# Kernel tuning notes

Measured on AMD Instinct MI355X. Metric: run time of the kernel, lower is better.

Reference implementation:

```python
import jax, jax.numpy as jnp
import numpy as np

N_NODES = 100000
N_EDGES = 6400000
N_ELEMENTS = 95  # covalent radii table size
P = 6  # envelope polynomial order (init kwarg p)


def setup_inputs() -> dict:
    key = jax.random.key(0)
    k1, k2, k3, k4 = jax.random.split(key, 4)
    z = jax.random.randint(k1, (N_NODES,), 1, 95)  # atomic numbers 1..94
    edge_distance = jax.random.uniform(k2, (N_EDGES,), jnp.float32, 0.5, 5.0)
    edge_index = jax.random.randint(k3, (2, N_EDGES), 0, N_NODES)
    covalent_radii = jax.random.uniform(k4, (N_ELEMENTS,), jnp.float32, 0.5, 2.0)
    return {
        "z": z,
        "edge_distance": edge_distance,
        "edge_index": edge_index,
        "a_factor": jnp.float32(0.4546),
        "Z_power": jnp.float32(0.0842),
        "screen_coefs": jnp.full((4,), 0.1663, jnp.float32),
        "screen_exps": jnp.full((4,), 0.0354, jnp.float32),
        "covalent_radii": covalent_radii,
    }


def reference(z, edge_distance, edge_index, a_factor, Z_power, screen_coefs, screen_exps, covalent_radii):
    sender, receiver = edge_index[0], edge_index[1]
    Z_u = z[sender]
    Z_v = z[receiver]
    Z_uf = Z_u.astype(edge_distance.dtype)
    Z_vf = Z_v.astype(edge_distance.dtype)

    # screening length a = a_factor * 0.529 / (Zu^zp + Zv^zp)
    a = a_factor * 0.529 / (Z_uf ** Z_power + Z_vf ** Z_power)
    r_over_a = edge_distance / a  # [E]

    # phi(x) = sum_i c_i * exp(-d_i * x)
    phi = jnp.sum(screen_coefs * jnp.exp(-screen_exps * r_over_a[:, None]), axis=-1)  # [E]

    v_edges = 14.3996 * Z_uf * Z_vf / edge_distance * phi

    # smooth cutoff envelope
    r_max = covalent_radii[Z_u] + covalent_radii[Z_v]
    t = edge_distance / r_max
    p = float(P)
    envelope = (1.0
                - (p + 1.0) * (p + 2.0) / 2.0 * t ** P
                + p * (p + 2.0) * t ** (P + 1)
                - p * (p + 1.0) / 2.0 * t ** (P + 2))
    envelope = envelope * (t < 1.0).astype(edge_distance.dtype)

    v_edges = 0.5 * v_edges * envelope

    # scatter-add per receiver node
    V_ZBL = jax.ops.segment_sum(v_edges, receiver, num_segments=z.shape[0])
    return V_ZBL
```

## Files before the change

### kernel.cpp

```cpp
#include <hip/hip_runtime.h>

#define N_ELEM 95
#define MAX_NODES 100096
#define ZW_WORDS (MAX_NODES / 4)
#define RS2 20480
#define MAX_R2 5
#define EBLK 256
#define CAP 4096

typedef float f32x4 __attribute__((ext_vector_type(4)));
typedef int   i32x4 __attribute__((ext_vector_type(4)));
typedef unsigned int u32;
typedef u32 u32x4 __attribute__((ext_vector_type(4)));
typedef unsigned long long u64;
typedef unsigned short u16;

__device__ __forceinline__ u32 bf16_rtn(float f) {
    u32 u = __float_as_uint(f);
    return (u + 0x7FFFu + ((u >> 16) & 1u)) >> 16;
}

__device__ __forceinline__ void build_ztab(
    u32* s_zw, const int* __restrict__ z, int n_words, int n_nodes, int tid, int nthr)
{
    for (int w = tid; w < n_words; w += nthr) {
        const int i = w << 2;
        u32 v;
        if (i + 4 <= n_nodes) {
            const i32x4 zz = ((const i32x4*)z)[w];
            v = ((u32)zz.x & 0xffu) | (((u32)zz.y & 0xffu) << 8)
              | (((u32)zz.z & 0xffu) << 16) | (((u32)zz.w & 0xffu) << 24);
        } else {
            v = 0u;
            for (int k = 0; k < 4 && i + k < n_nodes; ++k)
                v |= ((u32)z[i + k] & 0xffu) << (8 * k);
        }
        s_zw[w] = v;
    }
}

__global__ __launch_bounds__(1024) void k_edge_split(
    const int*   __restrict__ z,
    const float* __restrict__ dist,
    const int*   __restrict__ sender,
    const int*   __restrict__ recv,
    const float* __restrict__ a_factor_p,
    const float* __restrict__ z_power_p,
    const float* __restrict__ coefs,
    const float* __restrict__ exps,
    const float* __restrict__ cradii,
    u32*         __restrict__ seg,
    u32*         __restrict__ counts,
    float*       __restrict__ out,
    int n_edges, int n_words, int n_nodes, int W, int Rr)
{
    __shared__ u32    s_zw[ZW_WORDS];
    __shared__ float2 s_tab[N_ELEM];
    __shared__ float  s_coef[4], s_exp[4], s_inv;
    __shared__ u32    lcur[8];
    __shared__ u32    s_base[16][8];

    const int tid  = threadIdx.x;
    const int lane = tid & 63;
    const int wid  = tid >> 6;

    build_ztab(s_zw, z, n_words, n_nodes, tid, 1024);
    if (tid < N_ELEM) {
        float zp = z_power_p[0];
        s_tab[tid] = make_float2(__powf((float)tid, zp), cradii[tid]);
    }
    if (tid < 4) { s_coef[tid] = coefs[tid]; s_exp[tid] = exps[tid]; }
    if (tid < 8) lcur[tid] = 0u;
    if (tid == 0) s_inv = 1.0f / (a_factor_p[0] * 0.529f);
    __syncthreads();

    const unsigned char* s_zb = (const unsigned char*)s_zw;
    const float inv_pref = s_inv;
    const float c0 = s_coef[0], c1 = s_coef[1], c2 = s_coef[2], c3 = s_coef[3];
    const float e0 = s_exp[0],  e1 = s_exp[1],  e2 = s_exp[2],  e3 = s_exp[3];

    const int n_grp = n_edges >> 3;
    const int b     = blockIdx.x;
    const int g0    = b * W;
    const int g1    = min(n_grp, g0 + W);

    for (int gbase = g0; gbase < g1; gbase += 1024) {
        const int  gg     = gbase + tid;
        const bool active = (gg < g1);
        const int  g      = active ? gg : (g1 - 1);

        const f32x4 dA = ((const f32x4*)dist)[2 * g];
        const f32x4 dB = ((const f32x4*)dist)[2 * g + 1];
        const i32x4 sA = ((const i32x4*)sender)[2 * g];
        const i32x4 sB = ((const i32x4*)sender)[2 * g + 1];
        const i32x4 rA = ((const i32x4*)recv)[2 * g];
        const i32x4 rB = ((const i32x4*)recv)[2 * g + 1];

        float dd[8] = {dA.x, dA.y, dA.z, dA.w, dB.x, dB.y, dB.z, dB.w};
        int   ss[8] = {sA.x, sA.y, sA.z, sA.w, sB.x, sB.y, sB.z, sB.w};
        int   rr[8] = {rA.x, rA.y, rA.z, rA.w, rB.x, rB.y, rB.z, rB.w};

        int zu[8], zv[8];
        #pragma unroll
        for (int k = 0; k < 8; ++k) zu[k] = s_zb[ss[k]];
        #pragma unroll
        for (int k = 0; k < 8; ++k) zv[k] = s_zb[rr[k]];

        bool  em[8];
        float val[8];
        u32   entry[8], rgk[8];
        u64   cnt_pk = 0ull;

        #pragma unroll
        for (int k = 0; k < 8; ++k) {
            const float d = dd[k];
            const float2 tu = s_tab[zu[k]];
            const float2 tv = s_tab[zv[k]];
            const float rmax = tu.y + tv.y;
            em[k] = active && (d < rmax);
            float o = 0.0f;
            if (em[k]) {
                const float t   = __fdividef(d, rmax);
                const float roa = d * (tu.x + tv.x) * inv_pref;
                const float phi = c0 * __expf(-e0 * roa)
                                + c1 * __expf(-e1 * roa)
                                + c2 * __expf(-e2 * roa)
                                + c3 * __expf(-e3 * roa);
                const float v   = 7.1998f * (float)(zu[k] * zv[k]) * phi
                                * __fdividef(1.0f, d);
                const float t2  = t * t;
                const float t6  = t2 * t2 * t2;
                o = v * (1.0f - t6 * (28.0f - 48.0f * t + 21.0f * t2));
            }
            val[k] = o;
            const u32 rv  = (u32)rr[k];
            const u32 rg  = rv / (u32)RS2;
            rgk[k] = rg;
            entry[k] = ((rv - rg * (u32)RS2) << 16) | bf16_rtn(o);
            if (em[k]) cnt_pk += 1ull << (12 * rg);
        }

        u64 v = cnt_pk;
        #pragma unroll
        for (int d = 1; d < 64; d <<= 1) {
            u64 t = __shfl_up(v, (unsigned)d, 64);
            if (lane >= d) v += t;
        }
        const u64 excl = v - cnt_pk;

        if (lane == 63) {
            for (int r = 0; r < Rr; ++r) {
                const u32 tot = (u32)(v >> (12 * r)) & 0xFFFu;
                s_base[wid][r] = tot ? atomicAdd(&lcur[r], tot) : lcur[r];
            }
        }

        u64 run_pk = 0ull;
        #pragma unroll
        for (int k = 0; k < 8; ++k) {
            if (em[k]) {
                const u32 rg  = rgk[k];
                const u32 off = ((u32)(excl >> (12 * rg)) & 0xFFFu)
                              + ((u32)(run_pk >> (12 * rg)) & 0xFFFu);
                run_pk += 1ull << (12 * rg);
                const u32 base = s_base[wid][rg];
                const u32 pos  = base + off;
                if (pos < (u32)CAP)
                    seg[((size_t)b * Rr + rg) * CAP + pos] = entry[k];
                else
                    unsafeAtomicAdd(&out[rr[k]], val[k]);
            }
        }
    }

    if (b == gridDim.x - 1) {
        for (int i = (n_grp << 3) + tid; i < n_edges; i += 1024) {
            const float d  = dist[i];
            const int   a  = s_zb[sender[i]];
            const u32   rv = (u32)recv[i];
            const int   bb = s_zb[rv];
            const float2 tu = s_tab[a];
            const float2 tv = s_tab[bb];
            const float rmax = tu.y + tv.y;
            if (d < rmax) {
                const float t   = __fdividef(d, rmax);
                const float roa = d * (tu.x + tv.x) * inv_pref;
                const float phi = c0 * __expf(-e0 * roa)
                                + c1 * __expf(-e1 * roa)
                                + c2 * __expf(-e2 * roa)
                                + c3 * __expf(-e3 * roa);
                const float v   = 7.1998f * (float)(a * bb) * phi * __fdividef(1.0f, d);
                const float t2  = t * t;
                const float t6  = t2 * t2 * t2;
                const float o   = v * (1.0f - t6 * (28.0f - 48.0f * t + 21.0f * t2));
                const u32 rg    = rv / (u32)RS2;
                const u32 pos   = atomicAdd(&lcur[rg], 1u);
                if (pos < (u32)CAP)
                    seg[((size_t)b * Rr + rg) * CAP + pos] =
                        ((rv - rg * (u32)RS2) << 16) | bf16_rtn(o);
                else
                    unsafeAtomicAdd(&out[rv], o);
            }
        }
    }

    __syncthreads();
    if (tid < Rr)
        counts[b * Rr + tid] = min(lcur[tid], (u32)CAP);
}

__global__ __launch_bounds__(1024, 2) void k_gather_accum(
    const u32* __restrict__ seg,
    const u32* __restrict__ counts,
    u16*       __restrict__ copies,
    int C_acc, int Rr)
{
    __shared__ float acc[RS2];
    const int c = blockIdx.x % C_acc;
    const int r = blockIdx.x / C_acc;
    const int tid = threadIdx.x;

    int b0 = c;
    u32 cnt = (b0 < EBLK) ? counts[b0 * Rr + r] : 0u;

    for (int i = tid; i < RS2; i += 1024) acc[i] = 0.0f;
    __syncthreads();

    for (int b = c; b < EBLK; b += C_acc) {
        const int bn = b + C_acc;
        const u32 cnt_next = (bn < EBLK) ? counts[bn * Rr + r] : 0u;
        const u32* __restrict__ p = seg + ((size_t)b * Rr + r) * CAP;
        for (u32 i = tid; i < cnt; i += 1024) {
            const u32 w = p[i];
            atomicAdd(&acc[w >> 16], __uint_as_float((w & 0xFFFFu) << 16));
        }
        cnt = cnt_next;
    }
    __syncthreads();

    u16* __restrict__ dst = copies + ((size_t)c * Rr + r) * RS2;
    for (int i = tid * 8; i + 8 <= RS2; i += 8192) {
        const f32x4 a = *(const f32x4*)(acc + i);
        const f32x4 b = *(const f32x4*)(acc + i + 4);
        u32x4 o;
        o.x = bf16_rtn(a.x) | (bf16_rtn(a.y) << 16);
        o.y = bf16_rtn(a.z) | (bf16_rtn(a.w) << 16);
        o.z = bf16_rtn(b.x) | (bf16_rtn(b.y) << 16);
        o.w = bf16_rtn(b.z) | (bf16_rtn(b.w) << 16);
        *(u32x4*)(dst + i) = o;
    }
}

__global__ __launch_bounds__(256) void k_final5(
    const u32* __restrict__ copies32, float* __restrict__ out,
    int n_nodes, int C, int RRS32)
{
    const int p = blockIdx.x * 256 + threadIdx.x;
    const int n = p << 1;
    if (n < n_nodes) {
        float s0 = 0.0f, s1 = 0.0f;
        #pragma unroll 8
        for (int c = 0; c < C; ++c) {
            const u32 w = copies32[(size_t)c * RRS32 + p];
            s0 += __uint_as_float(w << 16);
            s1 += __uint_as_float(w & 0xFFFF0000u);
        }
        if (n + 1 < n_nodes) {
            const float2 prev = *(const float2*)(out + n);
            *(float2*)(out + n) = make_float2(prev.x + s0, prev.y + s1);
        } else {
            out[n] += s0;
        }
    }
}

__global__ __launch_bounds__(1024) void zbl_edge_lds(
    const int* __restrict__ z, const float* __restrict__ dist,
    const int* __restrict__ sender, const int* __restrict__ recv,
    const float* __restrict__ a_factor_p, const float* __restrict__ z_power_p,
    const float* __restrict__ coefs, const float* __restrict__ exps,
    const float* __restrict__ cradii, float* __restrict__ out,
    int n_edges, int n_words, int n_nodes)
{
    __shared__ u32    s_zw[ZW_WORDS];
    __shared__ float2 s_tab[N_ELEM];
    __shared__ float  s_coef[4], s_exp[4], s_inv;
    const int tid = threadIdx.x;
    build_ztab(s_zw, z, n_words, n_nodes, tid, 1024);
    if (tid < N_ELEM) {
        float zp = z_power_p[0];
        s_tab[tid] = make_float2(__powf((float)tid, zp), cradii[tid]);
    }
    if (tid < 4) { s_coef[tid] = coefs[tid]; s_exp[tid] = exps[tid]; }
    if (tid == 0) s_inv = 1.0f / (a_factor_p[0] * 0.529f);
    __syncthreads();
    const unsigned char* s_zb = (const unsigned char*)s_zw;
    const float inv_pref = s_inv;
    const int gstride = gridDim.x * 1024;
    for (int i = blockIdx.x * 1024 + tid; i < n_edges; i += gstride) {
        const float d  = dist[i];
        const int   a  = s_zb[sender[i]];
        const int   rv = recv[i];
        const int   b  = s_zb[rv];
        const float2 tu = s_tab[a];
        const float2 tv = s_tab[b];
        const float rmax = tu.y + tv.y;
        if (d < rmax) {
            const float t   = __fdividef(d, rmax);
            const float roa = d * (tu.x + tv.x) * inv_pref;
            const float phi = s_coef[0] * __expf(-s_exp[0] * roa)
                            + s_coef[1] * __expf(-s_exp[1] * roa)
                            + s_coef[2] * __expf(-s_exp[2] * roa)
                            + s_coef[3] * __expf(-s_exp[3] * roa);
            const float v   = 7.1998f * (float)(a * b) * phi * __fdividef(1.0f, d);
            const float t2  = t * t;
            const float t6  = t2 * t2 * t2;
            const float env = 1.0f - t6 * (28.0f - 48.0f * t + 21.0f * t2);
            unsafeAtomicAdd(&out[rv], v * env);
        }
    }
}

static inline size_t align16(size_t x) { return (x + 15) & ~(size_t)15; }

extern "C" void kernel_launch(void* const* d_in, const int* in_sizes, int n_in,
                              void* d_out, int out_size, void* d_ws, size_t ws_size,
                              hipStream_t stream) {
    const int*   z        = (const int*)d_in[0];
    const float* dist     = (const float*)d_in[1];
    const int*   eidx     = (const int*)d_in[2];
    const float* a_factor = (const float*)d_in[3];
    const float* z_power  = (const float*)d_in[4];
    const float* coefs    = (const float*)d_in[5];
    const float* exps     = (const float*)d_in[6];
    const float* cradii   = (const float*)d_in[7];
    float* out = (float*)d_out;

    const int n_edges = in_sizes[1];
    const int n_nodes = out_size;
    const int* sender = eidx;
    const int* recv   = eidx + n_edges;

    const int n_words = (n_nodes + 3) >> 2;
    const int R = (n_nodes + RS2 - 1) / RS2;

    const size_t seg_bytes = (size_t)EBLK * R * CAP * sizeof(u32);
    const size_t off_cnt   = align16(seg_bytes);
    const size_t off_cop   = align16(off_cnt + (size_t)EBLK * R * sizeof(u32));

    int C_acc = 0;
    if (R >= 1 && R <= MAX_R2 && n_nodes <= MAX_NODES) {
        const int opts[4] = {100, 51, 32, 16};
        for (int i = 0; i < 4; ++i) {
            size_t need = off_cop + (size_t)opts[i] * R * RS2 * sizeof(u16);
            if (ws_size >= need) { C_acc = opts[i]; break; }
        }
    }

    hipMemsetAsync(out, 0, (size_t)n_nodes * sizeof(float), stream);

    if (C_acc > 0) {
        char* ws = (char*)d_ws;
        u32* seg    = (u32*)ws;
        u32* counts = (u32*)(ws + off_cnt);
        u16* copies = (u16*)(ws + off_cop);

        const int n_grp = n_edges >> 3;
        const int W = (n_grp + EBLK - 1) / EBLK;

        k_edge_split<<<EBLK, 1024, 0, stream>>>(
            z, dist, sender, recv, a_factor, z_power, coefs, exps, cradii,
            seg, counts, out, n_edges, n_words, n_nodes, W, R);
        k_gather_accum<<<C_acc * R, 1024, 0, stream>>>(seg, counts, copies, C_acc, R);
        k_final5<<<((n_nodes + 1) / 2 + 255) / 256, 256, 0, stream>>>(
            (const u32*)copies, out, n_nodes, C_acc, (R * RS2) >> 1);
    } else if (n_nodes <= MAX_NODES) {
        zbl_edge_lds<<<256, 1024, 0, stream>>>(
            z, dist, sender, recv, a_factor, z_power, coefs, exps, cradii,
            out, n_edges, n_words, n_nodes);
    }
}
```

Measured before the change: 77.43 us.

## Shrink LDS z-table so two 1024-thread blocks fit per CU, double edge blocks

```diff
diff --git a/kernel.cpp b/kernel.cpp
--- a/kernel.cpp
+++ b/kernel.cpp
@@ -2,11 +2,12 @@
 
 #define N_ELEM 95
 #define MAX_NODES 100096
-#define ZW_WORDS (MAX_NODES / 4)
+#define ZSPLIT 80384
+#define ZW_WORDS (ZSPLIT / 4)
 #define RS2 20480
 #define MAX_R2 5
-#define EBLK 256
-#define CAP 4096
+#define EBLK 512
+#define CAP 2048
 
 typedef float f32x4 __attribute__((ext_vector_type(4)));
 typedef int   i32x4 __attribute__((ext_vector_type(4)));
@@ -21,9 +22,9 @@
 }
 
 __device__ __forceinline__ void build_ztab(
-    u32* s_zw, const int* __restrict__ z, int n_words, int n_nodes, int tid, int nthr)
-{
-    for (int w = tid; w < n_words; w += nthr) {
+    u32* s_zw, const int* __restrict__ z, int zw_words, int n_nodes, int tid, int nthr)
+{
+    for (int w = tid; w < zw_words; w += nthr) {
         const int i = w << 2;
         u32 v;
         if (i + 4 <= n_nodes) {
@@ -39,7 +40,7 @@
     }
 }
 
-__global__ __launch_bounds__(1024) void k_edge_split(
+__global__ __launch_bounds__(1024, 2) void k_edge_split(
     const int*   __restrict__ z,
     const float* __restrict__ dist,
     const int*   __restrict__ sender,
@@ -52,25 +53,25 @@
     u32*         __restrict__ seg,
     u32*         __restrict__ counts,
     float*       __restrict__ out,
-    int n_edges, int n_words, int n_nodes, int W, int Rr)
+    int n_edges, int zw_words, int n_nodes, int W, int Rr)
 {
     __shared__ u32    s_zw[ZW_WORDS];
     __shared__ float2 s_tab[N_ELEM];
     __shared__ float  s_coef[4], s_exp[4], s_inv;
-    __shared__ u32    lcur[8];
-    __shared__ u32    s_base[16][8];
+    __shared__ u32    lcur[MAX_R2];
+    __shared__ u32    s_base[16][MAX_R2];
 
     const int tid  = threadIdx.x;
     const int lane = tid & 63;
     const int wid  = tid >> 6;
 
-    build_ztab(s_zw, z, n_words, n_nodes, tid, 1024);
+    build_ztab(s_zw, z, zw_words, n_nodes, tid, 1024);
     if (tid < N_ELEM) {
         float zp = z_power_p[0];
         s_tab[tid] = make_float2(__powf((float)tid, zp), cradii[tid]);
     }
     if (tid < 4) { s_coef[tid] = coefs[tid]; s_exp[tid] = exps[tid]; }
-    if (tid < 8) lcur[tid] = 0u;
+    if (tid < MAX_R2) lcur[tid] = 0u;
     if (tid == 0) s_inv = 1.0f / (a_factor_p[0] * 0.529f);
     __syncthreads();
 
@@ -102,9 +103,15 @@
 
         int zu[8], zv[8];
         #pragma unroll
-        for (int k = 0; k < 8; ++k) zu[k] = s_zb[ss[k]];
-        #pragma unroll
-        for (int k = 0; k < 8; ++k) zv[k] = s_zb[rr[k]];
+        for (int k = 0; k < 8; ++k) {
+            const int i = ss[k];
+            zu[k] = (i < ZSPLIT) ? (int)s_zb[i] : z[i];
+        }
+        #pragma unroll
+        for (int k = 0; k < 8; ++k) {
+            const int i = rr[k];
+            zv[k] = (i < ZSPLIT) ? (int)s_zb[i] : z[i];
+        }
 
         bool  em[8];
         float val[8];
@@ -176,9 +183,10 @@
     if (b == gridDim.x - 1) {
         for (int i = (n_grp << 3) + tid; i < n_edges; i += 1024) {
             const float d  = dist[i];
-            const int   a  = s_zb[sender[i]];
+            const int   si = sender[i];
             const u32   rv = (u32)recv[i];
-            const int   bb = s_zb[rv];
+            const int   a  = (si < ZSPLIT) ? (int)s_zb[si] : z[si];
+            const int   bb = ((int)rv < ZSPLIT) ? (int)s_zb[rv] : z[rv];
             const float2 tu = s_tab[a];
             const float2 tv = s_tab[bb];
             const float rmax = tu.y + tv.y;
@@ -220,8 +228,7 @@
     const int r = blockIdx.x / C_acc;
     const int tid = threadIdx.x;
 
-    int b0 = c;
-    u32 cnt = (b0 < EBLK) ? counts[b0 * Rr + r] : 0u;
+    u32 cnt = (c < EBLK) ? counts[c * Rr + r] : 0u;
 
     for (int i = tid; i < RS2; i += 1024) acc[i] = 0.0f;
     __syncthreads();
@@ -274,19 +281,19 @@
     }
 }
 
-__global__ __launch_bounds__(1024) void zbl_edge_lds(
+__global__ __launch_bounds__(1024, 2) void zbl_edge_lds(
     const int* __restrict__ z, const float* __restrict__ dist,
     const int* __restrict__ sender, const int* __restrict__ recv,
     const float* __restrict__ a_factor_p, const float* __restrict__ z_power_p,
     const float* __restrict__ coefs, const float* __restrict__ exps,
     const float* __restrict__ cradii, float* __restrict__ out,
-    int n_edges, int n_words, int n_nodes)
+    int n_edges, int zw_words, int n_nodes)
 {
     __shared__ u32    s_zw[ZW_WORDS];
     __shared__ float2 s_tab[N_ELEM];
     __shared__ float  s_coef[4], s_exp[4], s_inv;
     const int tid = threadIdx.x;
-    build_ztab(s_zw, z, n_words, n_nodes, tid, 1024);
+    build_ztab(s_zw, z, zw_words, n_nodes, tid, 1024);
     if (tid < N_ELEM) {
         float zp = z_power_p[0];
         s_tab[tid] = make_float2(__powf((float)tid, zp), cradii[tid]);
@@ -299,9 +306,10 @@
     const int gstride = gridDim.x * 1024;
     for (int i = blockIdx.x * 1024 + tid; i < n_edges; i += gstride) {
         const float d  = dist[i];
-        const int   a  = s_zb[sender[i]];
+        const int   si = sender[i];
         const int   rv = recv[i];
-        const int   b  = s_zb[rv];
+        const int   a  = (si < ZSPLIT) ? (int)s_zb[si] : z[si];
+        const int   b  = (rv < ZSPLIT) ? (int)s_zb[rv] : z[rv];
         const float2 tu = s_tab[a];
         const float2 tv = s_tab[b];
         const float rmax = tu.y + tv.y;
@@ -341,7 +349,7 @@
     const int* sender = eidx;
     const int* recv   = eidx + n_edges;
 
-    const int n_words = (n_nodes + 3) >> 2;
+    const int zw_words = (min(n_nodes, ZSPLIT) + 3) >> 2;
     const int R = (n_nodes + RS2 - 1) / RS2;
 
     const size_t seg_bytes = (size_t)EBLK * R * CAP * sizeof(u32);
@@ -370,13 +378,13 @@
 
         k_edge_split<<<EBLK, 1024, 0, stream>>>(
             z, dist, sender, recv, a_factor, z_power, coefs, exps, cradii,
-            seg, counts, out, n_edges, n_words, n_nodes, W, R);
+            seg, counts, out, n_edges, zw_words, n_nodes, W, R);
         k_gather_accum<<<C_acc * R, 1024, 0, stream>>>(seg, counts, copies, C_acc, R);
         k_final5<<<((n_nodes + 1) / 2 + 255) / 256, 256, 0, stream>>>(
             (const u32*)copies, out, n_nodes, C_acc, (R * RS2) >> 1);
     } else if (n_nodes <= MAX_NODES) {
-        zbl_edge_lds<<<256, 1024, 0, stream>>>(
+        zbl_edge_lds<<<512, 1024, 0, stream>>>(
             z, dist, sender, recv, a_factor, z_power, coefs, exps, cradii,
-            out, n_edges, n_words, n_nodes);
-    }
-}
+            out, n_edges, zw_words, n_nodes);
+    }
+}
```

Measured after the change: 94.82 us. +22.5%, slower.

## Software-prefetch next edge group in split kernel and halve accumulator copies

Applied to the files above, without the earlier changes.

```diff
diff --git a/kernel.cpp b/kernel.cpp
--- a/kernel.cpp
+++ b/kernel.cpp
@@ -57,8 +57,8 @@
     __shared__ u32    s_zw[ZW_WORDS];
     __shared__ float2 s_tab[N_ELEM];
     __shared__ float  s_coef[4], s_exp[4], s_inv;
-    __shared__ u32    lcur[8];
-    __shared__ u32    s_base[16][8];
+    __shared__ u32    lcur[MAX_R2];
+    __shared__ u32    s_base[16][MAX_R2];
 
     const int tid  = threadIdx.x;
     const int lane = tid & 63;
@@ -70,7 +70,7 @@
         s_tab[tid] = make_float2(__powf((float)tid, zp), cradii[tid]);
     }
     if (tid < 4) { s_coef[tid] = coefs[tid]; s_exp[tid] = exps[tid]; }
-    if (tid < 8) lcur[tid] = 0u;
+    if (tid < MAX_R2) lcur[tid] = 0u;
     if (tid == 0) s_inv = 1.0f / (a_factor_p[0] * 0.529f);
     __syncthreads();
 
@@ -84,92 +84,107 @@
     const int g0    = b * W;
     const int g1    = min(n_grp, g0 + W);
 
-    for (int gbase = g0; gbase < g1; gbase += 1024) {
-        const int  gg     = gbase + tid;
-        const bool active = (gg < g1);
-        const int  g      = active ? gg : (g1 - 1);
-
-        const f32x4 dA = ((const f32x4*)dist)[2 * g];
-        const f32x4 dB = ((const f32x4*)dist)[2 * g + 1];
-        const i32x4 sA = ((const i32x4*)sender)[2 * g];
-        const i32x4 sB = ((const i32x4*)sender)[2 * g + 1];
-        const i32x4 rA = ((const i32x4*)recv)[2 * g];
-        const i32x4 rB = ((const i32x4*)recv)[2 * g + 1];
-
-        float dd[8] = {dA.x, dA.y, dA.z, dA.w, dB.x, dB.y, dB.z, dB.w};
-        int   ss[8] = {sA.x, sA.y, sA.z, sA.w, sB.x, sB.y, sB.z, sB.w};
-        int   rr[8] = {rA.x, rA.y, rA.z, rA.w, rB.x, rB.y, rB.z, rB.w};
-
-        int zu[8], zv[8];
-        #pragma unroll
-        for (int k = 0; k < 8; ++k) zu[k] = s_zb[ss[k]];
-        #pragma unroll
-        for (int k = 0; k < 8; ++k) zv[k] = s_zb[rr[k]];
-
-        bool  em[8];
-        float val[8];
-        u32   entry[8], rgk[8];
-        u64   cnt_pk = 0ull;
-
-        #pragma unroll
-        for (int k = 0; k < 8; ++k) {
-            const float d = dd[k];
-            const float2 tu = s_tab[zu[k]];
-            const float2 tv = s_tab[zv[k]];
-            const float rmax = tu.y + tv.y;
-            em[k] = active && (d < rmax);
-            float o = 0.0f;
-            if (em[k]) {
-                const float t   = __fdividef(d, rmax);
-                const float roa = d * (tu.x + tv.x) * inv_pref;
-                const float phi = c0 * __expf(-e0 * roa)
-                                + c1 * __expf(-e1 * roa)
-                                + c2 * __expf(-e2 * roa)
-                                + c3 * __expf(-e3 * roa);
-                const float v   = 7.1998f * (float)(zu[k] * zv[k]) * phi
-                                * __fdividef(1.0f, d);
-                const float t2  = t * t;
-                const float t6  = t2 * t2 * t2;
-                o = v * (1.0f - t6 * (28.0f - 48.0f * t + 21.0f * t2));
-            }
-            val[k] = o;
-            const u32 rv  = (u32)rr[k];
-            const u32 rg  = rv / (u32)RS2;
-            rgk[k] = rg;
-            entry[k] = ((rv - rg * (u32)RS2) << 16) | bf16_rtn(o);
-            if (em[k]) cnt_pk += 1ull << (12 * rg);
-        }
-
-        u64 v = cnt_pk;
-        #pragma unroll
-        for (int d = 1; d < 64; d <<= 1) {
-            u64 t = __shfl_up(v, (unsigned)d, 64);
-            if (lane >= d) v += t;
-        }
-        const u64 excl = v - cnt_pk;
-
-        if (lane == 63) {
-            for (int r = 0; r < Rr; ++r) {
-                const u32 tot = (u32)(v >> (12 * r)) & 0xFFFu;
-                s_base[wid][r] = tot ? atomicAdd(&lcur[r], tot) : lcur[r];
-            }
-        }
-
-        u64 run_pk = 0ull;
-        #pragma unroll
-        for (int k = 0; k < 8; ++k) {
-            if (em[k]) {
-                const u32 rg  = rgk[k];
-                const u32 off = ((u32)(excl >> (12 * rg)) & 0xFFFu)
-                              + ((u32)(run_pk >> (12 * rg)) & 0xFFFu);
-                run_pk += 1ull << (12 * rg);
-                const u32 base = s_base[wid][rg];
-                const u32 pos  = base + off;
-                if (pos < (u32)CAP)
-                    seg[((size_t)b * Rr + rg) * CAP + pos] = entry[k];
-                else
-                    unsafeAtomicAdd(&out[rr[k]], val[k]);
-            }
+    if (g0 < g1) {
+        const int n_iter = (g1 - g0 + 1023) >> 10;
+
+        int  gg  = g0 + tid;
+        bool act = (gg < g1);
+        int  g   = act ? gg : (g1 - 1);
+        f32x4 dA = ((const f32x4*)dist)[2 * g];
+        f32x4 dB = ((const f32x4*)dist)[2 * g + 1];
+        i32x4 sA = ((const i32x4*)sender)[2 * g];
+        i32x4 sB = ((const i32x4*)sender)[2 * g + 1];
+        i32x4 rA = ((const i32x4*)recv)[2 * g];
+        i32x4 rB = ((const i32x4*)recv)[2 * g + 1];
+
+        for (int it = 0; it < n_iter; ++it) {
+            const int  gg2  = gg + 1024;
+            const bool act2 = (gg2 < g1);
+            const int  g2   = act2 ? gg2 : (g1 - 1);
+            const f32x4 dA2 = ((const f32x4*)dist)[2 * g2];
+            const f32x4 dB2 = ((const f32x4*)dist)[2 * g2 + 1];
+            const i32x4 sA2 = ((const i32x4*)sender)[2 * g2];
+            const i32x4 sB2 = ((const i32x4*)sender)[2 * g2 + 1];
+            const i32x4 rA2 = ((const i32x4*)recv)[2 * g2];
+            const i32x4 rB2 = ((const i32x4*)recv)[2 * g2 + 1];
+
+            float dd[8] = {dA.x, dA.y, dA.z, dA.w, dB.x, dB.y, dB.z, dB.w};
+            int   ss[8] = {sA.x, sA.y, sA.z, sA.w, sB.x, sB.y, sB.z, sB.w};
+            int   rr[8] = {rA.x, rA.y, rA.z, rA.w, rB.x, rB.y, rB.z, rB.w};
+
+            int zu[8], zv[8];
+            #pragma unroll
+            for (int k = 0; k < 8; ++k) zu[k] = s_zb[ss[k]];
+            #pragma unroll
+            for (int k = 0; k < 8; ++k) zv[k] = s_zb[rr[k]];
+
+            bool  em[8];
+            float val[8];
+            u32   entry[8], rgk[8];
+            u64   cnt_pk = 0ull;
+
+            #pragma unroll
+            for (int k = 0; k < 8; ++k) {
+                const float d = dd[k];
+                const float2 tu = s_tab[zu[k]];
+                const float2 tv = s_tab[zv[k]];
+                const float rmax = tu.y + tv.y;
+                em[k] = act && (d < rmax);
+                float o = 0.0f;
+                if (em[k]) {
+                    const float t   = __fdividef(d, rmax);
+                    const float roa = d * (tu.x + tv.x) * inv_pref;
+                    const float phi = c0 * __expf(-e0 * roa)
+                                    + c1 * __expf(-e1 * roa)
+                                    + c2 * __expf(-e2 * roa)
+                                    + c3 * __expf(-e3 * roa);
+                    const float v   = 7.1998f * (float)(zu[k] * zv[k]) * phi
+                                    * __fdividef(1.0f, d);
+                    const float t2  = t * t;
+                    const float t6  = t2 * t2 * t2;
+                    o = v * (1.0f - t6 * (28.0f - 48.0f * t + 21.0f * t2));
+                }
+                val[k] = o;
+                const u32 rv  = (u32)rr[k];
+                const u32 rg  = rv / (u32)RS2;
+                rgk[k] = rg;
+                entry[k] = ((rv - rg * (u32)RS2) << 16) | bf16_rtn(o);
+                if (em[k]) cnt_pk += 1ull << (12 * rg);
+            }
+
+            u64 v = cnt_pk;
+            #pragma unroll
+            for (int d = 1; d < 64; d <<= 1) {
+                u64 t = __shfl_up(v, (unsigned)d, 64);
+                if (lane >= d) v += t;
+            }
+            const u64 excl = v - cnt_pk;
+
+            if (lane == 63) {
+                for (int r = 0; r < Rr; ++r) {
+                    const u32 tot = (u32)(v >> (12 * r)) & 0xFFFu;
+                    s_base[wid][r] = tot ? atomicAdd(&lcur[r], tot) : lcur[r];
+                }
+            }
+
+            u64 run_pk = 0ull;
+            #pragma unroll
+            for (int k = 0; k < 8; ++k) {
+                if (em[k]) {
+                    const u32 rg  = rgk[k];
+                    const u32 off = ((u32)(excl >> (12 * rg)) & 0xFFFu)
+                                  + ((u32)(run_pk >> (12 * rg)) & 0xFFFu);
+                    run_pk += 1ull << (12 * rg);
+                    const u32 pos = s_base[wid][rg] + off;
+                    if (pos < (u32)CAP)
+                        seg[((size_t)b * Rr + rg) * CAP + pos] = entry[k];
+                    else
+                        unsafeAtomicAdd(&out[rr[k]], val[k]);
+                }
+            }
+
+            dA = dA2; dB = dB2; sA = sA2; sB = sB2; rA = rA2; rB = rB2;
+            gg = gg2; act = act2;
         }
     }
 
@@ -220,8 +235,7 @@
     const int r = blockIdx.x / C_acc;
     const int tid = threadIdx.x;
 
-    int b0 = c;
-    u32 cnt = (b0 < EBLK) ? counts[b0 * Rr + r] : 0u;
+    u32 cnt = (c < EBLK) ? counts[c * Rr + r] : 0u;
 
     for (int i = tid; i < RS2; i += 1024) acc[i] = 0.0f;
     __syncthreads();
@@ -350,8 +364,8 @@
 
     int C_acc = 0;
     if (R >= 1 && R <= MAX_R2 && n_nodes <= MAX_NODES) {
-        const int opts[4] = {100, 51, 32, 16};
-        for (int i = 0; i < 4; ++i) {
+        const int opts[3] = {50, 32, 16};
+        for (int i = 0; i < 3; ++i) {
             size_t need = off_cop + (size_t)opts[i] * R * RS2 * sizeof(u16);
             if (ws_size >= need) { C_acc = opts[i]; break; }
         }
```

Result: faster. 75.28 us (-2.8%).
